# Optimization experiments

Measured on AMD Instinct MI355X. Metric: run time of the kernel, lower is better.

Reference implementation:

```python
import jax, jax.numpy as jnp
import numpy as np

B, K, D = 2, 2048, 1024
H, DQ, DV = 16, 64, 64
DFF = 4096
ATT_SIZE = 256
LN_EPS = 1e-5


def _layernorm(x, g, b):
    mu = jnp.mean(x, axis=-1, keepdims=True)
    var = jnp.mean(jnp.square(x - mu), axis=-1, keepdims=True)
    return (x - mu) * jax.lax.rsqrt(var + LN_EPS) * g + b


def setup_inputs() -> dict:
    key = jax.random.key(0)
    ks = jax.random.split(key, 16)
    s = lambda d: 1.0 / np.sqrt(d)
    return {
        "x": jax.random.normal(ks[0], (B, K, D), dtype=jnp.float32),
        "Wq": jax.random.normal(ks[1], (D, H * DQ), dtype=jnp.float32) * s(D),
        "bq": jnp.zeros((H * DQ,), dtype=jnp.float32),
        "Wk": jax.random.normal(ks[2], (D, H * DQ), dtype=jnp.float32) * s(D),
        "bk": jnp.zeros((H * DQ,), dtype=jnp.float32),
        "Wv": jax.random.normal(ks[3], (D, H * DV), dtype=jnp.float32) * s(D),
        "bv": jnp.zeros((H * DV,), dtype=jnp.float32),
        "Wo": jax.random.normal(ks[4], (H * DV, D), dtype=jnp.float32) * s(H * DV),
        "bo": jnp.zeros((D,), dtype=jnp.float32),
        "W1": jax.random.normal(ks[5], (D, DFF), dtype=jnp.float32) * s(D),
        "b1": jnp.zeros((DFF,), dtype=jnp.float32),
        "W2": jax.random.normal(ks[6], (DFF, D), dtype=jnp.float32) * s(DFF),
        "b2": jnp.zeros((D,), dtype=jnp.float32),
        "ln1_g": jnp.ones((D,), dtype=jnp.float32),
        "ln1_b": jnp.zeros((D,), dtype=jnp.float32),
        "ln2_g": jnp.ones((D,), dtype=jnp.float32),
        "ln2_b": jnp.zeros((D,), dtype=jnp.float32),
    }


def reference(x, Wq, bq, Wk, bk, Wv, bv, Wo, bo, W1, b1, W2, b2,
              ln1_g, ln1_b, ln2_g, ln2_b):
    b, k, d = x.shape
    # --- multi-head attention (heads formed by chunking last dim) ---
    q = (x @ Wq + bq).reshape(b, k, H, DQ)  # [b,k,h,dq]
    kk = (x @ Wk + bk).reshape(b, k, H, DQ)
    v = (x @ Wv + bv).reshape(b, k, H, DV)
    # NOTE: original scales by sqrt(K) (sequence length), not sqrt(d_q)
    scores = jnp.einsum('bshd,bthd->bhst', q, kk) / jnp.sqrt(jnp.float32(k))
    idx = jnp.arange(k)
    band_mask = jnp.abs(idx[:, None] - idx[None, :]) > ATT_SIZE  # [k,k] bool
    scores = jnp.where(band_mask[None, None], -jnp.inf, scores)
    attn = jax.nn.softmax(scores, axis=-1)
    ctx = jnp.einsum('bhst,bthd->bshd', attn, v).reshape(b, k, H * DV)
    sa = ctx @ Wo + bo
    x1 = _layernorm(sa + x, ln1_g, ln1_b)
    # --- position-wise FFN (exact GELU as torch F.gelu default) ---
    ff = (jax.nn.gelu(x1 @ W1 + b1, approximate=False)) @ W2 + b2
    return _layernorm(ff + x1, ln2_g, ln2_b)
```

## Files before the change

kernel.cpp:

```cpp
#include <hip/hip_runtime.h>
#include <cstdint>
#include <math.h>

typedef unsigned short u16;
typedef __attribute__((ext_vector_type(8))) short bf16x8;
typedef __attribute__((ext_vector_type(4))) float f32x4;

#define DEVI __device__ __forceinline__

DEVI u16 f2bf(float f) {
  union { float f; uint32_t u; } v; v.f = f;
  return (u16)((v.u + 0x7FFFu + ((v.u >> 16) & 1u)) >> 16);
}
DEVI float bf2f(u16 h) {
  union { uint32_t u; float f; } v; v.u = ((uint32_t)h) << 16;
  return v.f;
}

DEVI void gload16(const void* g, void* l) {
  __builtin_amdgcn_global_load_lds(
      (const __attribute__((address_space(1))) void*)g,
      (__attribute__((address_space(3))) void*)l, 16, 0, 0);
}

DEVI float gelu_fast(float u) {
  float u2 = u * u;
  float t = __builtin_fmaf(0.044715f * u2, u, u);
  float e = __expf(1.5957691216057308f * t);
  float r = __builtin_amdgcn_rcpf(1.0f + e);
  return u - u * r;
}

__global__ __launch_bounds__(256)
void cvt_kernel(const float* __restrict__ in, u16* __restrict__ out) {
  int i = (blockIdx.x * 256 + threadIdx.x) * 4;
  float4 f = *(const float4*)(in + i);
  uint32_t lo = (uint32_t)f2bf(f.x) | ((uint32_t)f2bf(f.y) << 16);
  uint32_t hi = (uint32_t)f2bf(f.z) | ((uint32_t)f2bf(f.w) << 16);
  *(uint2*)(out + i) = make_uint2(lo, hi);
}

__global__ __launch_bounds__(256)
void bcat_kernel(const float* __restrict__ bq, const float* __restrict__ bk,
                 const float* __restrict__ bv, float* __restrict__ out) {
  int i = blockIdx.x * 256 + threadIdx.x;
  const float* s = (i < 1024) ? bq : ((i < 2048) ? bk : bv);
  out[i] = s[i & 1023];
}

DEVI void tcvt_body(const float* __restrict__ W, u16* __restrict__ Wt,
                    int Kd, int N, int n0, int k0, float* t) {
  const int r = threadIdx.x >> 4, c4 = (threadIdx.x & 15) * 4;
#pragma unroll
  for (int p = 0; p < 4; ++p) {
    int row = p * 16 + r;
    float4 f = *(const float4*)(W + (size_t)(k0 + row) * N + n0 + c4);
    *(float4*)&t[row * 68 + c4] = f;
  }
  __syncthreads();
#pragma unroll
  for (int p = 0; p < 4; ++p) {
    int n = p * 16 + r;
    float v0 = t[(c4 + 0) * 68 + n];
    float v1 = t[(c4 + 1) * 68 + n];
    float v2 = t[(c4 + 2) * 68 + n];
    float v3 = t[(c4 + 3) * 68 + n];
    uint32_t lo = (uint32_t)f2bf(v0) | ((uint32_t)f2bf(v1) << 16);
    uint32_t hi = (uint32_t)f2bf(v2) | ((uint32_t)f2bf(v3) << 16);
    *(uint2*)(Wt + (size_t)(n0 + n) * Kd + k0 + c4) = make_uint2(lo, hi);
  }
}

__global__ __launch_bounds__(256)
void tcvt_kernel(const float* __restrict__ W, u16* __restrict__ Wt, int Kd, int N) {
  __shared__ float t[64 * 68];
  tcvt_body(W, Wt, Kd, N, blockIdx.x * 64, blockIdx.y * 64, t);
}

__global__ __launch_bounds__(256)
void tcvt4_kernel(const float* __restrict__ Wq, const float* __restrict__ Wk,
                  const float* __restrict__ Wv, const float* __restrict__ Wo,
                  u16* __restrict__ WqkvT, u16* __restrict__ WoT) {
  __shared__ float t[64 * 68];
  int z = blockIdx.z;
  const float* W = (z == 0) ? Wq : (z == 1) ? Wk : (z == 2) ? Wv : Wo;
  u16* dst = (z == 3) ? WoT : WqkvT + (size_t)z * 1024 * 1024;
  tcvt_body(W, dst, 1024, 1024, blockIdx.x * 64, blockIdx.y * 64, t);
}

template<int MODE>
__global__ __launch_bounds__(256)
void gemm_kernel(const u16* __restrict__ A, const u16* __restrict__ Bt,
                 const float* __restrict__ bias, void* __restrict__ C0,
                 void* __restrict__ C1, int N, int Kfull, int Kpart)
{
  __shared__ u16 As[128 * 32];
  __shared__ u16 Bs[128 * 32];
  const int tid = threadIdx.x;
  const int m0 = blockIdx.y * 128;
  const int n0 = blockIdx.x * 128;
  const int kbase = (MODE == 2) ? (int)blockIdx.z * Kpart : 0;
  const int w = tid >> 6, lane = tid & 63;
  const int wm = (w >> 1) * 64, wn = (w & 1) * 64;
  const int mr = lane & 15, ko = (lane >> 4) * 8;
  const int w32 = w * 32;

  f32x4 acc[4][4];
#pragma unroll
  for (int i = 0; i < 4; ++i)
#pragma unroll
    for (int j = 0; j < 4; ++j) {
      f32x4 z = {0.f, 0.f, 0.f, 0.f};
      acc[i][j] = z;
    }

  const int lr = lane >> 2, lk = (lane & 3) * 8;
  const u16* aG = A  + (size_t)(m0 + w32 + lr) * Kfull + kbase + lk;
  const u16* bG = Bt + (size_t)(n0 + w32 + lr) * Kfull + kbase + lk;
  u16* aL0 = &As[(w32 +  0) * 32];
  u16* aL1 = &As[(w32 + 16) * 32];
  u16* bL0 = &Bs[(w32 +  0) * 32];
  u16* bL1 = &Bs[(w32 + 16) * 32];
  const size_t row16 = (size_t)16 * Kfull;

  for (int k0 = 0; k0 < Kpart; k0 += 32) {
    gload16(aG + k0,         aL0);
    gload16(aG + row16 + k0, aL1);
    gload16(bG + k0,         bL0);
    gload16(bG + row16 + k0, bL1);
    __syncthreads();
    bf16x8 af[4], bf[4];
#pragma unroll
    for (int i = 0; i < 4; ++i)
      af[i] = *(const bf16x8*)&As[(wm + i * 16 + mr) * 32 + ko];
#pragma unroll
    for (int i = 0; i < 4; ++i)
      bf[i] = *(const bf16x8*)&Bs[(wn + i * 16 + mr) * 32 + ko];
#pragma unroll
    for (int i = 0; i < 4; ++i)
#pragma unroll
      for (int j = 0; j < 4; ++j)
        acc[i][j] = __builtin_amdgcn_mfma_f32_16x16x32_bf16(af[i], bf[j], acc[i][j], 0, 0, 0);
    __syncthreads();
  }

  const int rq = (lane >> 4) * 4;
  if (MODE == 0) {
    if (n0 < 2048) {
#pragma unroll
      for (int i = 0; i < 4; ++i) {
        int rbase = m0 + wm + i * 16 + rq;
#pragma unroll
        for (int j = 0; j < 4; ++j) {
          int col = n0 + wn + j * 16 + mr;
          float bv = bias[col];
#pragma unroll
          for (int r = 0; r < 4; ++r)
            ((u16*)C0)[(size_t)(rbase + r) * 2048 + col] = f2bf(acc[i][j][r] + bv);
        }
      }
    } else {
#pragma unroll
      for (int i = 0; i < 4; ++i) {
        int rbase = m0 + wm + i * 16 + rq;
#pragma unroll
        for (int j = 0; j < 4; ++j) {
          int col = n0 + wn + j * 16 + mr;
          float bv = bias[col];
          int d = col - 2048;
          uint32_t lo = (uint32_t)f2bf(acc[i][j][0] + bv) |
                        ((uint32_t)f2bf(acc[i][j][1] + bv) << 16);
          uint32_t hi = (uint32_t)f2bf(acc[i][j][2] + bv) |
                        ((uint32_t)f2bf(acc[i][j][3] + bv) << 16);
          *(uint2*)((u16*)C1 + (size_t)d * 4096 + rbase) = make_uint2(lo, hi);
        }
      }
    }
  } else {
    const bool part1 = (MODE == 2) && (blockIdx.z == 1);
#pragma unroll
    for (int i = 0; i < 4; ++i) {
      int rbase = m0 + wm + i * 16 + rq;
#pragma unroll
      for (int j = 0; j < 4; ++j) {
        int col = n0 + wn + j * 16 + mr;
        float bv = part1 ? 0.f : bias[col];
#pragma unroll
        for (int r = 0; r < 4; ++r) {
          float v = acc[i][j][r] + bv;
          if (MODE == 1) v = gelu_fast(v);
          size_t off = (size_t)(rbase + r) * N + col;
          if (MODE == 2) {
            if (part1) ((u16*)C1)[off] = f2bf(v);
            else       ((float*)C0)[off] = v;
          } else {
            ((u16*)C0)[off] = f2bf(v);
          }
        }
      }
    }
  }
}

__global__ __launch_bounds__(256)
void attn_kernel(const u16* __restrict__ QKb, const u16* __restrict__ Vt,
                 u16* __restrict__ ctx)
{
  const int KS = 2048, HD = 1024;
  __shared__ u16 Qs[64 * 80];
  __shared__ u16 Ks[64 * 80];
  __shared__ u16 Vts[64 * 72];
  __shared__ u16 Ps[64 * 72];

  const int qt = blockIdx.x, hh = blockIdx.y, bb = blockIdx.z;
  const int s0 = qt * 64;
  const int tid = threadIdx.x, w = tid >> 6, lane = tid & 63;
  const int quad = lane >> 4, mr = lane & 15;
  const int sr = tid >> 3, sc = (tid & 7) * 8;
  const int vrow = tid >> 2, vtc = (tid & 3) * 16;
  const float qsc = 0.022097086912079608f;

#pragma unroll
  for (int p = 0; p < 2; ++p) {
    int row = p * 32 + sr;
    uint4 u = *(const uint4*)(QKb + (size_t)(bb * KS + s0 + row) * 2048 + hh * 64 + sc);
    *(uint4*)&Qs[row * 80 + sc] = u;
  }

  f32x4 accO[4];
#pragma unroll
  for (int j = 0; j < 4; ++j) { f32x4 z = {0.f,0.f,0.f,0.f}; accO[j] = z; }
  float lsum[4] = {0.f, 0.f, 0.f, 0.f};

  for (int c = 0; c < 9; ++c) {
    int tb = s0 - 256 + c * 64;
    if (tb < 0 || tb >= KS) continue;
    __syncthreads();
#pragma unroll
    for (int p = 0; p < 2; ++p) {
      int row = p * 32 + sr;
      uint4 uk = *(const uint4*)(QKb + (size_t)(bb * KS + tb + row) * 2048 + 1024 + hh * 64 + sc);
      *(uint4*)&Ks[row * 80 + sc] = uk;
    }
    {
      const u16* vsrc = Vt + (size_t)(hh * 64 + vrow) * 4096 + bb * KS + tb + vtc;
      *(uint4*)&Vts[vrow * 72 + vtc]     = *(const uint4*)vsrc;
      *(uint4*)&Vts[vrow * 72 + vtc + 8] = *(const uint4*)(vsrc + 8);
    }
    __syncthreads();

    f32x4 sacc[4];
#pragma unroll
    for (int j = 0; j < 4; ++j) { f32x4 z = {0.f,0.f,0.f,0.f}; sacc[j] = z; }
#pragma unroll
    for (int s = 0; s < 2; ++s) {
      bf16x8 aq = *(const bf16x8*)&Qs[(w * 16 + mr) * 80 + s * 32 + quad * 8];
#pragma unroll
      for (int j = 0; j < 4; ++j) {
        bf16x8 bk = *(const bf16x8*)&Ks[(j * 16 + mr) * 80 + s * 32 + quad * 8];
        sacc[j] = __builtin_amdgcn_mfma_f32_16x16x32_bf16(aq, bk, sacc[j], 0, 0, 0);
      }
    }

#pragma unroll
    for (int r = 0; r < 4; ++r) {
      int qg = s0 + w * 16 + quad * 4 + r;
      int prow = (w * 16 + quad * 4 + r) * 72;
      float ls = 0.f;
#pragma unroll
      for (int j = 0; j < 4; ++j) {
        int tg = tb + j * 16 + mr;
        float s = sacc[j][r] * qsc;
        int d = qg - tg;
        if (d > 256 || d < -256) s = -INFINITY;
        float p = __expf(s);
        ls += p;
        Ps[prow + j * 16 + mr] = f2bf(p);
      }
      lsum[r] += ls;
    }
#pragma unroll
    for (int s = 0; s < 2; ++s) {
      bf16x8 ap = *(const bf16x8*)&Ps[(w * 16 + mr) * 72 + s * 32 + quad * 8];
#pragma unroll
      for (int j = 0; j < 4; ++j) {
        bf16x8 bv = *(const bf16x8*)&Vts[(j * 16 + mr) * 72 + s * 32 + quad * 8];
        accO[j] = __builtin_amdgcn_mfma_f32_16x16x32_bf16(ap, bv, accO[j], 0, 0, 0);
      }
    }
  }

#pragma unroll
  for (int r = 0; r < 4; ++r) {
    float l = lsum[r];
    l += __shfl_xor(l, 1, 64);
    l += __shfl_xor(l, 2, 64);
    l += __shfl_xor(l, 4, 64);
    l += __shfl_xor(l, 8, 64);
    int qg = s0 + w * 16 + quad * 4 + r;
    float inv = 1.f / l;
#pragma unroll
    for (int j = 0; j < 4; ++j) {
      int d = hh * 64 + j * 16 + mr;
      ctx[(size_t)(bb * KS + qg) * HD + d] = f2bf(accO[j][r] * inv);
    }
  }
}

template<int V>
__global__ __launch_bounds__(256)
void ln_kernel(const float* __restrict__ a, const u16* __restrict__ ab,
               const void* __restrict__ res, const float* __restrict__ g,
               const float* __restrict__ be, void* __restrict__ out)
{
  __shared__ float red[8];
  const int row = blockIdx.x, tid = threadIdx.x;
  const int w = tid >> 6, lane = tid & 63;
  size_t base = (size_t)row * 1024 + tid * 4;
  float4 va = *(const float4*)(a + base);
  float v0 = va.x, v1 = va.y, v2 = va.z, v3 = va.w;
  {
    uint2 u = *(const uint2*)(ab + base);
    v0 += bf2f((u16)(u.x & 0xFFFFu));
    v1 += bf2f((u16)(u.x >> 16));
    v2 += bf2f((u16)(u.y & 0xFFFFu));
    v3 += bf2f((u16)(u.y >> 16));
  }
  if (V == 0) {
    float4 vb = *(const float4*)((const float*)res + base);
    v0 += vb.x; v1 += vb.y; v2 += vb.z; v3 += vb.w;
  } else {
    uint2 u = *(const uint2*)((const u16*)res + base);
    v0 += bf2f((u16)(u.x & 0xFFFFu));
    v1 += bf2f((u16)(u.x >> 16));
    v2 += bf2f((u16)(u.y & 0xFFFFu));
    v3 += bf2f((u16)(u.y >> 16));
  }
  float s1 = v0 + v1 + v2 + v3;
  float s2 = v0 * v0 + v1 * v1 + v2 * v2 + v3 * v3;
#pragma unroll
  for (int o = 32; o > 0; o >>= 1) {
    s1 += __shfl_xor(s1, o, 64);
    s2 += __shfl_xor(s2, o, 64);
  }
  if (lane == 0) { red[w] = s1; red[4 + w] = s2; }
  __syncthreads();
  s1 = red[0] + red[1] + red[2] + red[3];
  s2 = red[4] + red[5] + red[6] + red[7];
  float mu = s1 * (1.f / 1024.f);
  float var = s2 * (1.f / 1024.f) - mu * mu;
  float rs = rsqrtf(var + 1e-5f);
  float4 gv = *(const float4*)(g + tid * 4);
  float4 bv = *(const float4*)(be + tid * 4);
  float o0 = (v0 - mu) * rs * gv.x + bv.x;
  float o1 = (v1 - mu) * rs * gv.y + bv.y;
  float o2 = (v2 - mu) * rs * gv.z + bv.z;
  float o3 = (v3 - mu) * rs * gv.w + bv.w;
  if (V == 0) {
    uint32_t lo = (uint32_t)f2bf(o0) | ((uint32_t)f2bf(o1) << 16);
    uint32_t hi = (uint32_t)f2bf(o2) | ((uint32_t)f2bf(o3) << 16);
    *(uint2*)((u16*)out + base) = make_uint2(lo, hi);
  } else {
    float4 ov; ov.x = o0; ov.y = o1; ov.z = o2; ov.w = o3;
    *(float4*)((float*)out + base) = ov;
  }
}

extern "C" void kernel_launch(void* const* d_in, const int* in_sizes, int n_in,
                              void* d_out, int out_size, void* d_ws, size_t ws_size,
                              hipStream_t stream)
{
  (void)in_sizes; (void)n_in; (void)out_size; (void)ws_size;
  const float* x   = (const float*)d_in[0];
  const float* Wq  = (const float*)d_in[1];
  const float* bq  = (const float*)d_in[2];
  const float* Wk  = (const float*)d_in[3];
  const float* bk  = (const float*)d_in[4];
  const float* Wv  = (const float*)d_in[5];
  const float* bv  = (const float*)d_in[6];
  const float* Wo  = (const float*)d_in[7];
  const float* bo  = (const float*)d_in[8];
  const float* W1  = (const float*)d_in[9];
  const float* b1  = (const float*)d_in[10];
  const float* W2  = (const float*)d_in[11];
  const float* b2  = (const float*)d_in[12];
  const float* g1  = (const float*)d_in[13];
  const float* be1 = (const float*)d_in[14];
  const float* g2  = (const float*)d_in[15];
  const float* be2 = (const float*)d_in[16];

  char* ws = (char*)d_ws;
  const size_t MB = 1048576;
  u16*   W1T   = (u16*)(ws + 0 * MB);
  u16*   Y1    = (u16*)(ws + 0 * MB);
  u16*   xb    = (u16*)(ws + 8 * MB);
  u16*   X1b   = (u16*)(ws + 8 * MB);
  u16*   WqkvT = (u16*)(ws + 16 * MB);
  u16*   WoT   = (u16*)(ws + 22 * MB);
  u16*   QKb   = (u16*)(ws + 24 * MB);
  float* SA0   = (float*)(ws + 24 * MB);
  u16*   Hb    = (u16*)(ws + 24 * MB);
  u16*   Vt    = (u16*)(ws + 40 * MB);
  u16*   SA1   = (u16*)(ws + 40 * MB);
  float* bqkv  = (float*)(ws + 48 * MB);
  u16*   Cb    = (u16*)(ws + 48 * MB);
  u16*   W2T   = (u16*)(ws + 56 * MB);
  float* yout  = (float*)d_out;

  dim3 blk(256);
  cvt_kernel<<<4096, blk, 0, stream>>>(x, xb);
  tcvt4_kernel<<<dim3(16, 16, 4), blk, 0, stream>>>(Wq, Wk, Wv, Wo, WqkvT, WoT);
  tcvt_kernel<<<dim3(64, 16), blk, 0, stream>>>(W1, W1T, 1024, 4096);
  tcvt_kernel<<<dim3(16, 64), blk, 0, stream>>>(W2, W2T, 4096, 1024);
  bcat_kernel<<<12, blk, 0, stream>>>(bq, bk, bv, bqkv);
  gemm_kernel<0><<<dim3(24, 32, 1), blk, 0, stream>>>(xb, WqkvT, bqkv, QKb, Vt, 3072, 1024, 1024);
  attn_kernel<<<dim3(32, 16, 2), blk, 0, stream>>>(QKb, Vt, Cb);
  gemm_kernel<2><<<dim3(8, 32, 2), blk, 0, stream>>>(Cb, WoT, bo, SA0, SA1, 1024, 1024, 512);
  ln_kernel<0><<<4096, blk, 0, stream>>>(SA0, SA1, x, g1, be1, X1b);
  gemm_kernel<1><<<dim3(32, 32, 1), blk, 0, stream>>>(X1b, W1T, b1, Hb, nullptr, 4096, 1024, 1024);
  gemm_kernel<2><<<dim3(8, 32, 2), blk, 0, stream>>>(Hb, W2T, b2, yout, Y1, 1024, 4096, 2048);
  ln_kernel<1><<<4096, blk, 0, stream>>>(yout, Y1, X1b, g2, be2, yout);
}
```

Baseline: 376.5 us.

## Merge prep kernels, widen GEMM K-step, swizzle block order, vectorize epilogue stores

Folds the five preprocessing launches (weight transpose-converts, x conversion, bias concat) into one prep kernel to cut launch overhead. The GEMM now stages 64 K-elements per barrier pair in two LDS buffers, remaps blocks into 8-row bands for L2 reuse, and sets launch bounds of 4 blocks per SM. MFMA operands are swapped so each lane holds four consecutive output columns, which allows packed vector stores of outputs and float4 bias loads. Attention gets the same operand swap, so softmax rows are reduced with two shuffles and ctx is written with packed stores. The transposed V output now uses scalar 2-byte stores, and the doubled LDS footprint may limit occupancy.

```diff
diff --git a/kernel.cpp b/kernel.cpp
--- a/kernel.cpp
+++ b/kernel.cpp
@@ -29,23 +29,6 @@
   float e = __expf(1.5957691216057308f * t);
   float r = __builtin_amdgcn_rcpf(1.0f + e);
   return u - u * r;
-}
-
-__global__ __launch_bounds__(256)
-void cvt_kernel(const float* __restrict__ in, u16* __restrict__ out) {
-  int i = (blockIdx.x * 256 + threadIdx.x) * 4;
-  float4 f = *(const float4*)(in + i);
-  uint32_t lo = (uint32_t)f2bf(f.x) | ((uint32_t)f2bf(f.y) << 16);
-  uint32_t hi = (uint32_t)f2bf(f.z) | ((uint32_t)f2bf(f.w) << 16);
-  *(uint2*)(out + i) = make_uint2(lo, hi);
-}
-
-__global__ __launch_bounds__(256)
-void bcat_kernel(const float* __restrict__ bq, const float* __restrict__ bk,
-                 const float* __restrict__ bv, float* __restrict__ out) {
-  int i = blockIdx.x * 256 + threadIdx.x;
-  const float* s = (i < 1024) ? bq : ((i < 2048) ? bk : bv);
-  out[i] = s[i & 1023];
 }
 
 DEVI void tcvt_body(const float* __restrict__ W, u16* __restrict__ Wt,
@@ -72,37 +55,62 @@
 }
 
 __global__ __launch_bounds__(256)
-void tcvt_kernel(const float* __restrict__ W, u16* __restrict__ Wt, int Kd, int N) {
+void prep_kernel(const float* __restrict__ Wq, const float* __restrict__ Wk,
+                 const float* __restrict__ Wv, const float* __restrict__ Wo,
+                 const float* __restrict__ W1, const float* __restrict__ W2,
+                 const float* __restrict__ x, const float* __restrict__ bq,
+                 const float* __restrict__ bk, const float* __restrict__ bv,
+                 u16* __restrict__ WqkvT, u16* __restrict__ WoT,
+                 u16* __restrict__ W1T, u16* __restrict__ W2T,
+                 u16* __restrict__ xb, float* __restrict__ bqkv)
+{
   __shared__ float t[64 * 68];
-  tcvt_body(W, Wt, Kd, N, blockIdx.x * 64, blockIdx.y * 64, t);
-}
-
-__global__ __launch_bounds__(256)
-void tcvt4_kernel(const float* __restrict__ Wq, const float* __restrict__ Wk,
-                  const float* __restrict__ Wv, const float* __restrict__ Wo,
-                  u16* __restrict__ WqkvT, u16* __restrict__ WoT) {
-  __shared__ float t[64 * 68];
-  int z = blockIdx.z;
-  const float* W = (z == 0) ? Wq : (z == 1) ? Wk : (z == 2) ? Wv : Wo;
-  u16* dst = (z == 3) ? WoT : WqkvT + (size_t)z * 1024 * 1024;
-  tcvt_body(W, dst, 1024, 1024, blockIdx.x * 64, blockIdx.y * 64, t);
+  const int b = blockIdx.x;
+  if (b < 1024) {
+    int wsel = b >> 8, tt = b & 255;
+    const float* W = (wsel == 0) ? Wq : (wsel == 1) ? Wk : (wsel == 2) ? Wv : Wo;
+    u16* dst = (wsel == 3) ? WoT : WqkvT + (size_t)wsel * 1024 * 1024;
+    tcvt_body(W, dst, 1024, 1024, (tt & 15) * 64, (tt >> 4) * 64, t);
+  } else if (b < 2048) {
+    int tt = b - 1024;
+    tcvt_body(W1, W1T, 1024, 4096, (tt & 63) * 64, (tt >> 6) * 64, t);
+  } else if (b < 3072) {
+    int tt = b - 2048;
+    tcvt_body(W2, W2T, 4096, 1024, (tt & 15) * 64, (tt >> 4) * 64, t);
+  } else if (b < 7168) {
+    int i = ((b - 3072) * 256 + threadIdx.x) * 4;
+    float4 f = *(const float4*)(x + i);
+    uint32_t lo = (uint32_t)f2bf(f.x) | ((uint32_t)f2bf(f.y) << 16);
+    uint32_t hi = (uint32_t)f2bf(f.z) | ((uint32_t)f2bf(f.w) << 16);
+    *(uint2*)(xb + i) = make_uint2(lo, hi);
+  } else {
+    int i = (b - 7168) * 256 + threadIdx.x;
+    const float* s = (i < 1024) ? bq : ((i < 2048) ? bk : bv);
+    bqkv[i] = s[i & 1023];
+  }
 }
 
 template<int MODE>
-__global__ __launch_bounds__(256)
+__global__ __launch_bounds__(256, 4)
 void gemm_kernel(const u16* __restrict__ A, const u16* __restrict__ Bt,
                  const float* __restrict__ bias, void* __restrict__ C0,
                  void* __restrict__ C1, int N, int Kfull, int Kpart)
 {
-  __shared__ u16 As[128 * 32];
-  __shared__ u16 Bs[128 * 32];
+  __shared__ u16 As0[128 * 32], As1[128 * 32];
+  __shared__ u16 Bs0[128 * 32], Bs1[128 * 32];
   const int tid = threadIdx.x;
-  const int m0 = blockIdx.y * 128;
-  const int n0 = blockIdx.x * 128;
+  const int nbx = gridDim.x, nby = gridDim.y;
+  int lin = blockIdx.y * nbx + blockIdx.x;
+  int band = lin / (8 * nbx);
+  int rem = lin - band * (8 * nbx);
+  int gsz = min(nby - band * 8, 8);
+  const int m0 = (band * 8 + rem % gsz) * 128;
+  const int n0 = (rem / gsz) * 128;
   const int kbase = (MODE == 2) ? (int)blockIdx.z * Kpart : 0;
   const int w = tid >> 6, lane = tid & 63;
   const int wm = (w >> 1) * 64, wn = (w & 1) * 64;
   const int mr = lane & 15, ko = (lane >> 4) * 8;
+  const int rq = (lane >> 4) * 4;
   const int w32 = w * 32;
 
   f32x4 acc[4][4];
@@ -117,62 +125,75 @@
   const int lr = lane >> 2, lk = (lane & 3) * 8;
   const u16* aG = A  + (size_t)(m0 + w32 + lr) * Kfull + kbase + lk;
   const u16* bG = Bt + (size_t)(n0 + w32 + lr) * Kfull + kbase + lk;
-  u16* aL0 = &As[(w32 +  0) * 32];
-  u16* aL1 = &As[(w32 + 16) * 32];
-  u16* bL0 = &Bs[(w32 +  0) * 32];
-  u16* bL1 = &Bs[(w32 + 16) * 32];
+  u16* aD00 = &As0[(w32 +  0) * 32];
+  u16* aD01 = &As0[(w32 + 16) * 32];
+  u16* aD10 = &As1[(w32 +  0) * 32];
+  u16* aD11 = &As1[(w32 + 16) * 32];
+  u16* bD00 = &Bs0[(w32 +  0) * 32];
+  u16* bD01 = &Bs0[(w32 + 16) * 32];
+  u16* bD10 = &Bs1[(w32 +  0) * 32];
+  u16* bD11 = &Bs1[(w32 + 16) * 32];
   const size_t row16 = (size_t)16 * Kfull;
 
-  for (int k0 = 0; k0 < Kpart; k0 += 32) {
-    gload16(aG + k0,         aL0);
-    gload16(aG + row16 + k0, aL1);
-    gload16(bG + k0,         bL0);
-    gload16(bG + row16 + k0, bL1);
+  for (int k0 = 0; k0 < Kpart; k0 += 64) {
+    gload16(aG + k0,              aD00);
+    gload16(aG + row16 + k0,      aD01);
+    gload16(aG + k0 + 32,         aD10);
+    gload16(aG + row16 + k0 + 32, aD11);
+    gload16(bG + k0,              bD00);
+    gload16(bG + row16 + k0,      bD01);
+    gload16(bG + k0 + 32,         bD10);
+    gload16(bG + row16 + k0 + 32, bD11);
     __syncthreads();
-    bf16x8 af[4], bf[4];
-#pragma unroll
-    for (int i = 0; i < 4; ++i)
-      af[i] = *(const bf16x8*)&As[(wm + i * 16 + mr) * 32 + ko];
-#pragma unroll
-    for (int i = 0; i < 4; ++i)
-      bf[i] = *(const bf16x8*)&Bs[(wn + i * 16 + mr) * 32 + ko];
-#pragma unroll
-    for (int i = 0; i < 4; ++i)
+#pragma unroll
+    for (int s = 0; s < 2; ++s) {
+      const u16* Ap = s ? As1 : As0;
+      const u16* Bp = s ? Bs1 : Bs0;
+      bf16x8 af[4], bf[4];
+#pragma unroll
+      for (int i = 0; i < 4; ++i)
+        af[i] = *(const bf16x8*)&Ap[(wm + i * 16 + mr) * 32 + ko];
 #pragma unroll
       for (int j = 0; j < 4; ++j)
-        acc[i][j] = __builtin_amdgcn_mfma_f32_16x16x32_bf16(af[i], bf[j], acc[i][j], 0, 0, 0);
+        bf[j] = *(const bf16x8*)&Bp[(wn + j * 16 + mr) * 32 + ko];
+#pragma unroll
+      for (int i = 0; i < 4; ++i)
+#pragma unroll
+        for (int j = 0; j < 4; ++j)
+          acc[i][j] = __builtin_amdgcn_mfma_f32_16x16x32_bf16(bf[j], af[i], acc[i][j], 0, 0, 0);
+    }
     __syncthreads();
   }
 
-  const int rq = (lane >> 4) * 4;
   if (MODE == 0) {
     if (n0 < 2048) {
 #pragma unroll
       for (int i = 0; i < 4; ++i) {
-        int rbase = m0 + wm + i * 16 + rq;
+        size_t mrow = (size_t)(m0 + wm + i * 16 + mr) * 2048;
 #pragma unroll
         for (int j = 0; j < 4; ++j) {
-          int col = n0 + wn + j * 16 + mr;
-          float bv = bias[col];
-#pragma unroll
-          for (int r = 0; r < 4; ++r)
-            ((u16*)C0)[(size_t)(rbase + r) * 2048 + col] = f2bf(acc[i][j][r] + bv);
+          int nb = n0 + wn + j * 16 + rq;
+          float4 b4 = *(const float4*)&bias[nb];
+          uint32_t lo = (uint32_t)f2bf(acc[i][j][0] + b4.x) |
+                        ((uint32_t)f2bf(acc[i][j][1] + b4.y) << 16);
+          uint32_t hi = (uint32_t)f2bf(acc[i][j][2] + b4.z) |
+                        ((uint32_t)f2bf(acc[i][j][3] + b4.w) << 16);
+          *(uint2*)((u16*)C0 + mrow + nb) = make_uint2(lo, hi);
         }
       }
     } else {
 #pragma unroll
       for (int i = 0; i < 4; ++i) {
-        int rbase = m0 + wm + i * 16 + rq;
+        int mg = m0 + wm + i * 16 + mr;
 #pragma unroll
         for (int j = 0; j < 4; ++j) {
-          int col = n0 + wn + j * 16 + mr;
-          float bv = bias[col];
-          int d = col - 2048;
-          uint32_t lo = (uint32_t)f2bf(acc[i][j][0] + bv) |
-                        ((uint32_t)f2bf(acc[i][j][1] + bv) << 16);
-          uint32_t hi = (uint32_t)f2bf(acc[i][j][2] + bv) |
-                        ((uint32_t)f2bf(acc[i][j][3] + bv) << 16);
-          *(uint2*)((u16*)C1 + (size_t)d * 4096 + rbase) = make_uint2(lo, hi);
+          int nb = n0 + wn + j * 16 + rq;
+          float4 b4 = *(const float4*)&bias[nb];
+          int d = nb - 2048;
+          ((u16*)C1)[(size_t)(d + 0) * 4096 + mg] = f2bf(acc[i][j][0] + b4.x);
+          ((u16*)C1)[(size_t)(d + 1) * 4096 + mg] = f2bf(acc[i][j][1] + b4.y);
+          ((u16*)C1)[(size_t)(d + 2) * 4096 + mg] = f2bf(acc[i][j][2] + b4.z);
+          ((u16*)C1)[(size_t)(d + 3) * 4096 + mg] = f2bf(acc[i][j][3] + b4.w);
         }
       }
     }
@@ -180,22 +201,31 @@
     const bool part1 = (MODE == 2) && (blockIdx.z == 1);
 #pragma unroll
     for (int i = 0; i < 4; ++i) {
-      int rbase = m0 + wm + i * 16 + rq;
+      size_t mrow = (size_t)(m0 + wm + i * 16 + mr) * N;
 #pragma unroll
       for (int j = 0; j < 4; ++j) {
-        int col = n0 + wn + j * 16 + mr;
-        float bv = part1 ? 0.f : bias[col];
-#pragma unroll
-        for (int r = 0; r < 4; ++r) {
-          float v = acc[i][j][r] + bv;
-          if (MODE == 1) v = gelu_fast(v);
-          size_t off = (size_t)(rbase + r) * N + col;
-          if (MODE == 2) {
-            if (part1) ((u16*)C1)[off] = f2bf(v);
-            else       ((float*)C0)[off] = v;
-          } else {
-            ((u16*)C0)[off] = f2bf(v);
-          }
+        int nb = n0 + wn + j * 16 + rq;
+        if (MODE == 1) {
+          float4 b4 = *(const float4*)&bias[nb];
+          float v0 = gelu_fast(acc[i][j][0] + b4.x);
+          float v1 = gelu_fast(acc[i][j][1] + b4.y);
+          float v2 = gelu_fast(acc[i][j][2] + b4.z);
+          float v3 = gelu_fast(acc[i][j][3] + b4.w);
+          uint32_t lo = (uint32_t)f2bf(v0) | ((uint32_t)f2bf(v1) << 16);
+          uint32_t hi = (uint32_t)f2bf(v2) | ((uint32_t)f2bf(v3) << 16);
+          *(uint2*)((u16*)C0 + mrow + nb) = make_uint2(lo, hi);
+        } else if (part1) {
+          uint32_t lo = (uint32_t)f2bf(acc[i][j][0]) | ((uint32_t)f2bf(acc[i][j][1]) << 16);
+          uint32_t hi = (uint32_t)f2bf(acc[i][j][2]) | ((uint32_t)f2bf(acc[i][j][3]) << 16);
+          *(uint2*)((u16*)C1 + mrow + nb) = make_uint2(lo, hi);
+        } else {
+          float4 b4 = *(const float4*)&bias[nb];
+          float4 ov;
+          ov.x = acc[i][j][0] + b4.x;
+          ov.y = acc[i][j][1] + b4.y;
+          ov.z = acc[i][j][2] + b4.z;
+          ov.w = acc[i][j][3] + b4.w;
+          *(float4*)((float*)C0 + mrow + nb) = ov;
         }
       }
     }
@@ -215,10 +245,11 @@
   const int qt = blockIdx.x, hh = blockIdx.y, bb = blockIdx.z;
   const int s0 = qt * 64;
   const int tid = threadIdx.x, w = tid >> 6, lane = tid & 63;
-  const int quad = lane >> 4, mr = lane & 15;
+  const int mr = lane & 15, ko = (lane >> 4) * 8, rq = (lane >> 4) * 4;
   const int sr = tid >> 3, sc = (tid & 7) * 8;
   const int vrow = tid >> 2, vtc = (tid & 3) * 16;
   const float qsc = 0.022097086912079608f;
+  const int qg = s0 + w * 16 + mr;
 
 #pragma unroll
   for (int p = 0; p < 2; ++p) {
@@ -230,7 +261,7 @@
   f32x4 accO[4];
 #pragma unroll
   for (int j = 0; j < 4; ++j) { f32x4 z = {0.f,0.f,0.f,0.f}; accO[j] = z; }
-  float lsum[4] = {0.f, 0.f, 0.f, 0.f};
+  float lsum = 0.f;
 
   for (int c = 0; c < 9; ++c) {
     int tb = s0 - 256 + c * 64;
@@ -254,56 +285,55 @@
     for (int j = 0; j < 4; ++j) { f32x4 z = {0.f,0.f,0.f,0.f}; sacc[j] = z; }
 #pragma unroll
     for (int s = 0; s < 2; ++s) {
-      bf16x8 aq = *(const bf16x8*)&Qs[(w * 16 + mr) * 80 + s * 32 + quad * 8];
+      bf16x8 aq = *(const bf16x8*)&Qs[(w * 16 + mr) * 80 + s * 32 + ko];
 #pragma unroll
       for (int j = 0; j < 4; ++j) {
-        bf16x8 bk = *(const bf16x8*)&Ks[(j * 16 + mr) * 80 + s * 32 + quad * 8];
-        sacc[j] = __builtin_amdgcn_mfma_f32_16x16x32_bf16(aq, bk, sacc[j], 0, 0, 0);
-      }
-    }
-
-#pragma unroll
-    for (int r = 0; r < 4; ++r) {
-      int qg = s0 + w * 16 + quad * 4 + r;
-      int prow = (w * 16 + quad * 4 + r) * 72;
-      float ls = 0.f;
+        bf16x8 bk = *(const bf16x8*)&Ks[(j * 16 + mr) * 80 + s * 32 + ko];
+        sacc[j] = __builtin_amdgcn_mfma_f32_16x16x32_bf16(bk, aq, sacc[j], 0, 0, 0);
+      }
+    }
+
+#pragma unroll
+    for (int j = 0; j < 4; ++j) {
+      int tgb = tb + j * 16 + rq;
+      float p0, p1, p2, p3;
+      {
+        int d0 = qg - tgb;
+        float s_ = sacc[j][0] * qsc;
+        p0 = (d0 > 256 || d0 < -256) ? 0.f : __expf(s_);
+        int d1 = d0 - 1; s_ = sacc[j][1] * qsc;
+        p1 = (d1 > 256 || d1 < -256) ? 0.f : __expf(s_);
+        int d2 = d0 - 2; s_ = sacc[j][2] * qsc;
+        p2 = (d2 > 256 || d2 < -256) ? 0.f : __expf(s_);
+        int d3 = d0 - 3; s_ = sacc[j][3] * qsc;
+        p3 = (d3 > 256 || d3 < -256) ? 0.f : __expf(s_);
+      }
+      lsum += p0 + p1 + p2 + p3;
+      uint32_t lo = (uint32_t)f2bf(p0) | ((uint32_t)f2bf(p1) << 16);
+      uint32_t hi = (uint32_t)f2bf(p2) | ((uint32_t)f2bf(p3) << 16);
+      *(uint2*)&Ps[(w * 16 + mr) * 72 + j * 16 + rq] = make_uint2(lo, hi);
+    }
+#pragma unroll
+    for (int s = 0; s < 2; ++s) {
+      bf16x8 ap = *(const bf16x8*)&Ps[(w * 16 + mr) * 72 + s * 32 + ko];
 #pragma unroll
       for (int j = 0; j < 4; ++j) {
-        int tg = tb + j * 16 + mr;
-        float s = sacc[j][r] * qsc;
-        int d = qg - tg;
-        if (d > 256 || d < -256) s = -INFINITY;
-        float p = __expf(s);
-        ls += p;
-        Ps[prow + j * 16 + mr] = f2bf(p);
-      }
-      lsum[r] += ls;
-    }
-#pragma unroll
-    for (int s = 0; s < 2; ++s) {
-      bf16x8 ap = *(const bf16x8*)&Ps[(w * 16 + mr) * 72 + s * 32 + quad * 8];
-#pragma unroll
-      for (int j = 0; j < 4; ++j) {
-        bf16x8 bv = *(const bf16x8*)&Vts[(j * 16 + mr) * 72 + s * 32 + quad * 8];
-        accO[j] = __builtin_amdgcn_mfma_f32_16x16x32_bf16(ap, bv, accO[j], 0, 0, 0);
-      }
-    }
-  }
-
-#pragma unroll
-  for (int r = 0; r < 4; ++r) {
-    float l = lsum[r];
-    l += __shfl_xor(l, 1, 64);
-    l += __shfl_xor(l, 2, 64);
-    l += __shfl_xor(l, 4, 64);
-    l += __shfl_xor(l, 8, 64);
-    int qg = s0 + w * 16 + quad * 4 + r;
-    float inv = 1.f / l;
-#pragma unroll
-    for (int j = 0; j < 4; ++j) {
-      int d = hh * 64 + j * 16 + mr;
-      ctx[(size_t)(bb * KS + qg) * HD + d] = f2bf(accO[j][r] * inv);
-    }
+        bf16x8 bv = *(const bf16x8*)&Vts[(j * 16 + mr) * 72 + s * 32 + ko];
+        accO[j] = __builtin_amdgcn_mfma_f32_16x16x32_bf16(bv, ap, accO[j], 0, 0, 0);
+      }
+    }
+  }
+
+  float l = lsum;
+  l += __shfl_xor(l, 16, 64);
+  l += __shfl_xor(l, 32, 64);
+  float inv = 1.f / l;
+  size_t base = (size_t)(bb * KS + qg) * HD + hh * 64;
+#pragma unroll
+  for (int j = 0; j < 4; ++j) {
+    uint32_t lo = (uint32_t)f2bf(accO[j][0] * inv) | ((uint32_t)f2bf(accO[j][1] * inv) << 16);
+    uint32_t hi = (uint32_t)f2bf(accO[j][2] * inv) | ((uint32_t)f2bf(accO[j][3] * inv) << 16);
+    *(uint2*)(ctx + base + j * 16 + rq) = make_uint2(lo, hi);
   }
 }
 
@@ -408,11 +438,8 @@
   float* yout  = (float*)d_out;
 
   dim3 blk(256);
-  cvt_kernel<<<4096, blk, 0, stream>>>(x, xb);
-  tcvt4_kernel<<<dim3(16, 16, 4), blk, 0, stream>>>(Wq, Wk, Wv, Wo, WqkvT, WoT);
-  tcvt_kernel<<<dim3(64, 16), blk, 0, stream>>>(W1, W1T, 1024, 4096);
-  tcvt_kernel<<<dim3(16, 64), blk, 0, stream>>>(W2, W2T, 4096, 1024);
-  bcat_kernel<<<12, blk, 0, stream>>>(bq, bk, bv, bqkv);
+  prep_kernel<<<7180, blk, 0, stream>>>(Wq, Wk, Wv, Wo, W1, W2, x, bq, bk, bv,
+                                        WqkvT, WoT, W1T, W2T, xb, bqkv);
   gemm_kernel<0><<<dim3(24, 32, 1), blk, 0, stream>>>(xb, WqkvT, bqkv, QKb, Vt, 3072, 1024, 1024);
   attn_kernel<<<dim3(32, 16, 2), blk, 0, stream>>>(QKb, Vt, Cb);
   gemm_kernel<2><<<dim3(8, 32, 2), blk, 0, stream>>>(Cb, WoT, bo, SA0, SA1, 1024, 1024, 512);
```

Result: faster. 327.4 us (-13.0%).
